# Optimization experiments

Measured on AMD Instinct MI355X. Metric: run time of the kernel, lower is better.

The kernel has to match this reference:

```python
import jax, jax.numpy as jnp
import numpy as np

L = 14  # max_relative_position
H = 12  # num_heads
HD = 64  # head_dim


def rel_pos_embed(N, table_v, table_h):
    # 2D relative-position embedding with a leading CLS token (index 0).
    n = N - 1
    s = int(n ** 0.5)  # grid side (14)
    r = jnp.arange(n)
    dv = r[None, :] // s - r[:, None] // s  # vertical distance
    dh = r[None, :] % s - r[:, None] % s   # horizontal distance
    iv = jnp.clip(dv, -L, L) + L + 1
    ih = jnp.clip(dh, -L, L) + L + 1
    iv = jnp.pad(iv, ((1, 0), (1, 0)))  # CLS row/col -> index 0
    ih = jnp.pad(ih, ((1, 0), (1, 0)))
    return table_v[iv] + table_h[ih]  # [N, N, HD]


def setup_inputs() -> dict:
    key = jax.random.key(0)
    ks = jax.random.split(key, 11)
    B, N, E = 64, 197, 768
    T = 2 * L + 2  # rel-pos table rows (30)
    std = 0.02
    return {
        "x": jax.random.normal(ks[0], (B, N, E), jnp.float32),
        "wq": jax.random.normal(ks[1], (E, H * HD), jnp.float32) * std,
        "wk": jax.random.normal(ks[2], (E, H * HD), jnp.float32) * std,
        "wv": jax.random.normal(ks[3], (E, H * HD), jnp.float32) * std,
        "wproj": jax.random.normal(ks[4], (H * HD, E), jnp.float32) * std,
        "bproj": jnp.zeros((E,), jnp.float32),
        "rk_v": jax.random.normal(ks[5], (T, HD), jnp.float32) * std,
        "rk_h": jax.random.normal(ks[6], (T, HD), jnp.float32) * std,
        "rv_v": jax.random.normal(ks[7], (T, HD), jnp.float32) * std,
        "rv_h": jax.random.normal(ks[8], (T, HD), jnp.float32) * std,
    }


def reference(x, wq, wk, wv, wproj, bproj, rk_v, rk_h, rv_v, rv_h):
    B, N, E = x.shape
    scale = HD ** -0.5
    q = (x @ wq).reshape(B, N, H, HD).transpose(0, 2, 1, 3)  # [B,H,N,HD]
    k = (x @ wk).reshape(B, N, H, HD).transpose(0, 2, 1, 3)
    v = (x @ wv).reshape(B, N, H, HD).transpose(0, 2, 1, 3)

    attn = jnp.einsum('bhid,bhjd->bhij', q, k) * scale
    rpk = rel_pos_embed(N, rk_v, rk_h)  # [N,N,HD]
    attn = attn + jnp.einsum('bhid,ijd->bhij', q, rpk) * scale
    attn = jax.nn.softmax(attn, axis=-1)

    out = jnp.einsum('bhij,bhjd->bhid', attn, v)
    rpv = rel_pos_embed(N, rv_v, rv_h)
    out = out + jnp.einsum('bhij,ijd->bhid', attn, rpv)

    out = out.transpose(0, 2, 1, 3).reshape(B, N, H * HD)
    return out @ wproj + bproj
```

## Files before the change

### kernel.cpp

```cpp
#include <hip/hip_runtime.h>
#include <math.h>

typedef _Float16 f16;
typedef __attribute__((ext_vector_type(8))) _Float16 f16x8;
typedef __attribute__((ext_vector_type(4))) _Float16 f16x4;
typedef __attribute__((ext_vector_type(4))) float f32x4;

#define NH 12
#define HDIM 64
#define NTOK 197
#define EDIM 768
#define NB 64
#define MROWS (NB*NTOK)

__device__ __forceinline__ void wfence() {
    asm volatile("s_waitcnt lgkmcnt(0)" ::: "memory");
    __builtin_amdgcn_sched_barrier(0);
    __builtin_amdgcn_wave_barrier();
}

__device__ __forceinline__ unsigned div14(unsigned n) { return (n * 4682u) >> 16; }

__device__ __forceinline__ void gload16(const f16* g, f16* lds_base) {
    __builtin_amdgcn_global_load_lds(
        (const __attribute__((address_space(1))) void*)g,
        (__attribute__((address_space(3))) void*)lds_base, 16, 0, 0);
}

__global__ __launch_bounds__(256) void prep_all(
    const float* __restrict__ x,
    const float* __restrict__ wq, const float* __restrict__ wk,
    const float* __restrict__ wv, const float* __restrict__ wp,
    const float* __restrict__ rkv, const float* __restrict__ rkh,
    f16* __restrict__ xh, f16* __restrict__ wqkvT, f16* __restrict__ wpT,
    f16* __restrict__ gA, f16* __restrict__ gt_buf)
{
    __shared__ float T[64][65];
    const int bid = blockIdx.x;
    if (bid < 4728) {
        int idx = bid * 256 + threadIdx.x;
        const float4* s = (const float4*)x + (size_t)idx * 2;
        float4 a = s[0], b = s[1];
        f16x8 h;
        h[0]=(f16)a.x; h[1]=(f16)a.y; h[2]=(f16)a.z; h[3]=(f16)a.w;
        h[4]=(f16)b.x; h[5]=(f16)b.y; h[6]=(f16)b.z; h[7]=(f16)b.w;
        *(f16x8*)(xh + (size_t)idx * 8) = h;
    } else if (bid < 5304) {
        int b2 = bid - 4728;
        int m = b2 / 144, rem = b2 - m*144;
        const float* src = (m==0)?wq:(m==1)?wk:(m==2)?wv:wp;
        int k0 = (rem / 12) * 64, n0 = (rem % 12) * 64;
        int cidx = threadIdx.x & 63, r4 = threadIdx.x >> 6;
#pragma unroll
        for (int rr = 0; rr < 16; ++rr) {
            int kl = rr*4 + r4;
            T[kl][cidx] = src[(size_t)(k0+kl)*EDIM + n0 + cidx];
        }
        __syncthreads();
        f16* dst = (m < 3) ? (wqkvT + (size_t)m*EDIM*EDIM) : wpT;
#pragma unroll
        for (int rr = 0; rr < 16; ++rr) {
            int nl = rr*4 + r4;
            dst[(size_t)(n0+nl)*EDIM + k0 + cidx] = (f16)T[cidx][nl];
        }
    } else {
        int t = (bid - 5304) * 256 + threadIdx.x;
        const int stride = 32 * 256;
        for (int i = t; i < 272*128; i += stride) {
            int row = i >> 7, cs = i & 127;
            int c = cs ^ ((row & 7) << 3);
            f16 v = (f16)0.f;
            if (c < 64) {
                if (row >= 208 && row < 238)      v = (f16)rkv[(row-208)*64 + c];
                else if (row >= 240 && row < 270) v = (f16)rkh[(row-240)*64 + c];
            } else if (c < 96 && row < 208) {
                int g = c - 64;
                if (row == 0) { if (g == 14 || g == 30) v = (f16)1.f; }
                else if (row <= 196) {
                    int rm = row - 1;
                    int gv = (int)div14((unsigned)rm), gh = rm - gv*14;
                    if (g == gv || g == 16 + gh) v = (f16)1.f;
                }
            }
            gA[i] = v;
        }
        for (int i = t; i < 32*256; i += stride) {
            int g = i >> 8, cs = i & 255;
            int j = cs ^ ((g & 7) << 3);
            f16 v = (f16)0.f;
            if (j >= 1 && j <= 196) {
                int jm = j - 1;
                int gv = (int)div14((unsigned)jm), gh = jm - gv*14;
                if ((g < 14 && gv == g) || (g >= 16 && g < 30 && gh == g - 16))
                    v = (f16)1.f;
            }
            gt_buf[i] = v;
        }
    }
}

__global__ __launch_bounds__(512, 2) void gemm256(
    const f16* __restrict__ A, const f16* __restrict__ Bt,
    f16* __restrict__ q_o, f16* __restrict__ k_o, f16* __restrict__ v_o,
    float* __restrict__ p_o, const float* __restrict__ bias, int mode, int nxb)
{
    __shared__ f16 lds[2*16384];

    const int tid = threadIdx.x;
    const int l = tid & 63, w = tid >> 6;
    const int lr = l & 15, lq = l >> 4;
    const int wr = w >> 2, wc = w & 3;

    const int nwg = gridDim.x, orig = blockIdx.x;
    const int xcd = orig & 7, qc = nwg >> 3, rc = nwg & 7;
    const int wgid = (xcd < rc ? xcd*(qc+1) : rc*(qc+1) + (xcd-rc)*qc) + (orig >> 3);
    const int mband = wgid / nxb, nband = wgid - mband*nxb;
    const int m0 = mband << 8, n0 = nband << 8;

    const int scol = (((tid & 7) ^ ((tid >> 3) & 7)) << 3);
    const f16* aG[4]; const f16* bG[4];
#pragma unroll
    for (int p = 0; p < 4; ++p) {
        int rt = p*64 + (tid >> 3);
        int ra = m0 + rt; if (ra >= MROWS) ra = MROWS - 1;
        aG[p] = A  + (size_t)ra * EDIM + scol;
        bG[p] = Bt + (size_t)(n0 + rt) * EDIM + scol;
    }
    const int lbase = w * 512;

    f32x4 acc[8][4];
#pragma unroll
    for (int mt = 0; mt < 8; ++mt)
#pragma unroll
        for (int nt = 0; nt < 4; ++nt) {
            acc[mt][nt][0]=0.f; acc[mt][nt][1]=0.f;
            acc[mt][nt][2]=0.f; acc[mt][nt][3]=0.f;
        }

#pragma unroll
    for (int p = 0; p < 4; ++p) {
        gload16(aG[p], &lds[p*4096 + lbase]);
        gload16(bG[p], &lds[16384 + p*4096 + lbase]);
    }
    asm volatile("s_waitcnt vmcnt(0)" ::: "memory");
    __builtin_amdgcn_sched_barrier(0);
    __builtin_amdgcn_s_barrier();

    const int swz = (lr & 7) << 3;
    for (int kt = 0; kt < 12; ++kt) {
        __builtin_amdgcn_s_setprio(1);
#pragma unroll
        for (int ks = 0; ks < 2; ++ks) {
            const int kb = (ks*32 + lq*8) ^ swz;
            f16x8 bf[4];
#pragma unroll
            for (int nt = 0; nt < 4; ++nt)
                bf[nt] = *(const f16x8*)&lds[16384 + (wc*64 + nt*16 + lr)*64 + kb];
#pragma unroll
            for (int mt = 0; mt < 8; ++mt) {
                f16x8 af = *(const f16x8*)&lds[(wr*128 + mt*16 + lr)*64 + kb];
#pragma unroll
                for (int nt = 0; nt < 4; ++nt)
                    acc[mt][nt] = __builtin_amdgcn_mfma_f32_16x16x32_f16(
                        af, bf[nt], acc[mt][nt], 0, 0, 0);
            }
        }
        __builtin_amdgcn_s_setprio(0);
        __builtin_amdgcn_s_barrier();
        if (kt < 11) {
            const int ko = (kt + 1) * 64;
#pragma unroll
            for (int p = 0; p < 4; ++p) {
                gload16(aG[p] + ko, &lds[p*4096 + lbase]);
                gload16(bG[p] + ko, &lds[16384 + p*4096 + lbase]);
            }
            asm volatile("s_waitcnt vmcnt(0)" ::: "memory");
            __builtin_amdgcn_sched_barrier(0);
            __builtin_amdgcn_s_barrier();
        }
    }

    if (mode == 0) {
        const int mat   = n0 / EDIM;
        const int hbase = ((n0 % EDIM) >> 6) + wc;
        f16* dst = (mat == 0) ? q_o : (mat == 1) ? k_o : v_o;
        f16* scr = &lds[w * 2304];
#pragma unroll
        for (int mt2 = 0; mt2 < 4; ++mt2) {
#pragma unroll
            for (int mtp = 0; mtp < 2; ++mtp) {
                const int mt = mt2*2 + mtp;
#pragma unroll
                for (int nt = 0; nt < 4; ++nt)
#pragma unroll
                    for (int rg = 0; rg < 4; ++rg)
                        scr[(mtp*16 + lq*4 + rg)*72 + nt*16 + lr] = (f16)acc[mt][nt][rg];
            }
            wfence();
#pragma unroll
            for (int i = 0; i < 4; ++i) {
                int row = (l >> 3) + i*8;
                f16x8 v = *(const f16x8*)&scr[row*72 + (l & 7)*8];
                int R = m0 + wr*128 + mt2*32 + row;
                if (R < MROWS) {
                    int bb = R / NTOK, nn = R - bb*NTOK;
                    *(f16x8*)&dst[((size_t)(bb*NH + hbase)*NTOK + nn)*HDIM + (l & 7)*8] = v;
                }
            }
            wfence();
        }
    } else {
#pragma unroll
        for (int mt = 0; mt < 8; ++mt)
#pragma unroll
            for (int rg = 0; rg < 4; ++rg) {
                int R = m0 + wr*128 + mt*16 + lq*4 + rg;
                if (R < MROWS) {
                    float* base = p_o + (size_t)R * EDIM + n0 + wc*64;
#pragma unroll
                    for (int nt = 0; nt < 4; ++nt) {
                        int c = nt*16 + lr;
                        base[c] = acc[mt][nt][rg] + bias[n0 + wc*64 + c];
                    }
                }
            }
    }
}

#define SKE 128
#define SVT 320
#define SGT 256
#define SWS 72
#define ATHR 832

__global__ __launch_bounds__(ATHR, 1) void attn_mfma(
    const f16* __restrict__ q_ws, const f16* __restrict__ k_ws,
    const f16* __restrict__ v_ws,
    const float* __restrict__ rvv, const float* __restrict__ rvh,
    const f16* __restrict__ gA, const f16* __restrict__ gt_buf,
    f16* __restrict__ o_ws)
{
    __shared__ f16 Kle[272*SKE];
    __shared__ f16 Vt[64*SVT];
    __shared__ f16 Gt[32*SGT];
    __shared__ f16 WSh[13*16*SWS];

    const int tid = threadIdx.x;
    const int w = tid >> 6, l = tid & 63;
    const int lr = l & 15, lq = l >> 4;
    const int bh = blockIdx.x;
    const int b = bh / NH, h = bh - b * NH;
    const f16* Qp = q_ws + (size_t)bh * NTOK * HDIM;
    const f16* Kp = k_ws + (size_t)bh * NTOK * HDIM;
    const f16* Vp = v_ws + (size_t)bh * NTOK * HDIM;
    f16* wsh = &WSh[w * 16 * SWS];

    for (int c = w; c < 84; c += 13) {
        f16* ldsb;
        const f16* gsrc;
        if (c < 68) {
            int idx = c*64 + l;
            int row = idx >> 4, cs8 = (idx & 15) << 3;
            ldsb = &Kle[c * 512];
            gsrc = (row < NTOK && cs8 < 64)
                 ? (Kp + row*64 + (cs8 ^ ((row & 7) << 3)))
                 : (gA + row*SKE + cs8);
        } else {
            int c2 = c - 68;
            ldsb = &Gt[c2 * 512];
            gsrc = gt_buf + c2*512 + l*8;
        }
        gload16(gsrc, ldsb);
    }

    f16x8 vbuf[4];
#pragma unroll
    for (int it = 0; it < 4; ++it) {
        int idx = tid + it*ATHR;
        if (idx < 8*SVT) {
            int dlow = idx & 7, k = idx >> 3;
            bool isV = (k < NTOK), isA = (k >= 208 && k < 238), isB = (k >= 238 && k < 268);
#pragma unroll
            for (int e = 0; e < 8; ++e) {
                int d = (e << 3) + dlow;
                f16 val = (f16)0.f;
                if (isV)      val = Vp[k*64 + d];
                else if (isA) val = (f16)rvv[(k-208)*64 + d];
                else if (isB) val = (f16)rvh[(k-238)*64 + d];
                vbuf[it][e] = val;
            }
        }
    }

    const int tt = w;
    const int i0 = tt * 16;
    const int iq = i0 + lr;
    const int iqc = (iq > 196) ? 196 : iq;
    const f16* qsrc = Qp + iqc*64 + lq*8;
    f16x8 qf0 = *(const f16x8*)qsrc;
    f16x8 qf1 = *(const f16x8*)(qsrc + 32);

    __syncthreads();

    const int src0 = ((l >> 4) & 1) * 32 + lr;
    const int src1 = src0 + 16;
    const int sw = (lr & 7) << 3;

    {
        __builtin_amdgcn_s_setprio(1);
        f32x4 pacc[4];
#pragma unroll
        for (int ct = 0; ct < 4; ++ct) {
            f32x4 a; a[0]=0.f; a[1]=0.f; a[2]=0.f; a[3]=0.f;
            const int krow = (13+ct)*16 + lr;
            f16x8 kf0 = *(f16x8*)&Kle[krow*SKE + ((lq*8) ^ sw)];
            f16x8 kf1 = *(f16x8*)&Kle[krow*SKE + ((32 + lq*8) ^ sw)];
            a = __builtin_amdgcn_mfma_f32_16x16x32_f16(kf0, qf0, a, 0, 0, 0);
            a = __builtin_amdgcn_mfma_f32_16x16x32_f16(kf1, qf1, a, 0, 0, 0);
            pacc[ct] = a;
        }
        __builtin_amdgcn_s_setprio(0);
#pragma unroll
        for (int ct = 0; ct < 4; ++ct)
#pragma unroll
            for (int rg = 0; rg < 4; ++rg)
                wsh[lr*SWS + ct*16 + lq*4 + rg] = (f16)pacc[ct][rg];
        wfence();

        int id_ = 0, ih_ = 0;
        const bool qcls = (iq == 0);
        if (iq > 0) { unsigned v = div14((unsigned)(iq-1)); id_ = (int)v; ih_ = (iq-1) - (int)v*14; }
        f16x8 qcf;
#pragma unroll
        for (int e = 0; e < 8; ++e) {
            int g = lq*8 + e;
            int toff;
            if (g < 14)       toff = qcls ? 0 : (g - id_ + 15);
            else if (g == 14) toff = 0;
            else if (g == 15) toff = 63;
            else if (g < 30)  toff = qcls ? 32 : (32 + (g-16) - ih_ + 15);
            else if (g == 30) toff = 32;
            else              toff = 63;
            qcf[e] = wsh[lr*SWS + toff];
        }

        f32x4 acc[13];
        __builtin_amdgcn_s_setprio(1);
#pragma unroll
        for (int ct = 0; ct < 13; ++ct) {
            f32x4 a; a[0]=0.f; a[1]=0.f; a[2]=0.f; a[3]=0.f;
            const int krow = ct*16 + lr;
            f16x8 kf0 = *(f16x8*)&Kle[krow*SKE + ((lq*8) ^ sw)];
            f16x8 kf1 = *(f16x8*)&Kle[krow*SKE + ((32 + lq*8) ^ sw)];
            f16x8 gf  = *(f16x8*)&Kle[krow*SKE + ((64 + lq*8) ^ sw)];
            a = __builtin_amdgcn_mfma_f32_16x16x32_f16(kf0, qf0, a, 0, 0, 0);
            a = __builtin_amdgcn_mfma_f32_16x16x32_f16(kf1, qf1, a, 0, 0, 0);
            a = __builtin_amdgcn_mfma_f32_16x16x32_f16(gf,  qcf, a, 0, 0, 0);
            acc[ct] = a;
        }
        __builtin_amdgcn_s_setprio(0);

#pragma unroll
        for (int rg = 0; rg < 4; ++rg)
            if (lq*4 + rg > 4) acc[12][rg] = -1e30f;

        float m = -1e30f;
#pragma unroll
        for (int ct = 0; ct < 13; ++ct)
#pragma unroll
            for (int rg = 0; rg < 4; ++rg) m = fmaxf(m, acc[ct][rg]);
        m = fmaxf(m, __shfl_xor(m, 16));
        m = fmaxf(m, __shfl_xor(m, 32));
        const float C1 = 0.125f * 1.44269504088896f;
        const float nm = -m * C1;
        float ssum = 0.f;
#pragma unroll
        for (int ct = 0; ct < 13; ++ct)
#pragma unroll
            for (int rg = 0; rg < 4; ++rg) {
                float p = exp2f(fmaf(acc[ct][rg], C1, nm));
                acc[ct][rg] = p; ssum += p;
            }
        ssum += __shfl_xor(ssum, 16);
        ssum += __shfl_xor(ssum, 32);
        const float inv = 1.f / ssum;
        const float pn00 = acc[0][0] * inv;

        unsigned pk[13][2];
#pragma unroll
        for (int ct = 0; ct < 13; ++ct) {
            union { f16x4 hh; unsigned u[2]; } t;
            t.hh[0] = (f16)(acc[ct][0] * inv);
            t.hh[1] = (f16)(acc[ct][1] * inv);
            t.hh[2] = (f16)(acc[ct][2] * inv);
            t.hh[3] = (f16)(acc[ct][3] * inv);
            pk[ct][0] = t.u[0]; pk[ct][1] = t.u[1];
        }

        f16x8 pa[7];
#pragma unroll
        for (int kc = 0; kc < 7; ++kc) {
            const int ctA = 2*kc;
            const int ctB = (kc == 6) ? 12 : 2*kc + 1;
            unsigned A0 = (unsigned)__shfl((int)pk[ctA][0], src0);
            unsigned A1 = (unsigned)__shfl((int)pk[ctA][1], src0);
            unsigned A2 = (unsigned)__shfl((int)pk[ctA][0], src1);
            unsigned A3 = (unsigned)__shfl((int)pk[ctA][1], src1);
            unsigned B0 = (unsigned)__shfl((int)pk[ctB][0], src0);
            unsigned B1 = (unsigned)__shfl((int)pk[ctB][1], src0);
            unsigned B2 = (unsigned)__shfl((int)pk[ctB][0], src1);
            unsigned B3 = (unsigned)__shfl((int)pk[ctB][1], src1);
            bool hiHalf = (lq >= 2);
            union { unsigned u[4]; f16x8 v; } f;
            f.u[0] = hiHalf ? B0 : A0;
            f.u[1] = hiHalf ? B1 : A1;
            f.u[2] = hiHalf ? B2 : A2;
            f.u[3] = hiHalf ? B3 : A3;
            if (kc == 6 && hiHalf) { f.u[0]=0; f.u[1]=0; f.u[2]=0; f.u[3]=0; }
            pa[kc] = f.v;
        }

        f32x4 gacc[2];
#pragma unroll
        for (int ct = 0; ct < 2; ++ct) { gacc[ct][0]=0.f; gacc[ct][1]=0.f; gacc[ct][2]=0.f; gacc[ct][3]=0.f; }
        __builtin_amdgcn_s_setprio(1);
#pragma unroll
        for (int kc = 0; kc < 7; ++kc) {
#pragma unroll
            for (int ct = 0; ct < 2; ++ct) {
                f16x8 gf = *(f16x8*)&Gt[(ct*16 + lr)*SGT + ((kc*32 + lq*8) ^ sw)];
                gacc[ct] = __builtin_amdgcn_mfma_f32_16x16x32_f16(pa[kc], gf, gacc[ct], 0, 0, 0);
            }
        }
        __builtin_amdgcn_s_setprio(0);

#pragma unroll
        for (int z = 0; z < 2; ++z) {
            int zi = z*64 + l;
            int zr = zi >> 3, zc = (zi & 7) << 3;
            f16x8 zz;
#pragma unroll
            for (int e = 0; e < 8; ++e) zz[e] = (f16)0.f;
            *(f16x8*)&wsh[zr*SWS + zc] = zz;
        }
        wfence();
#pragma unroll
        for (int rg = 0; rg < 4; ++rg) {
            int il = lq*4 + rg;
            int is_ = i0 + il;
            if (lr < 14 && is_ > 0) {
                unsigned v = div14((unsigned)(is_-1));
                int id2 = (int)v, ih2 = (is_-1) - (int)v*14;
                wsh[il*SWS + (lr - id2 + 15)]      = (f16)gacc[0][rg];
                wsh[il*SWS + 30 + (lr - ih2 + 15)] = (f16)gacc[1][rg];
            }
        }
        if (lq == 0 && !(i0 == 0 && lr == 0)) {
            wsh[lr*SWS + 0]  = (f16)pn00;
            wsh[lr*SWS + 30] = (f16)pn00;
        }
        if (i0 == 0) {
            float sv = (lq == 0) ? gacc[0][0] : 0.f;
            float sh = (lq == 0) ? gacc[1][0] : 0.f;
            sv += __shfl_xor(sv, 1); sv += __shfl_xor(sv, 2);
            sv += __shfl_xor(sv, 4); sv += __shfl_xor(sv, 8);
            sh += __shfl_xor(sh, 1); sh += __shfl_xor(sh, 2);
            sh += __shfl_xor(sh, 4); sh += __shfl_xor(sh, 8);
            if (l == 0) {
                wsh[0]  = (f16)(sv + pn00);
                wsh[30] = (f16)(sh + pn00);
            }
        }
        wfence();

#pragma unroll
        for (int it = 0; it < 4; ++it) {
            int idx = tid + it*ATHR;
            if (idx < 8*SVT) {
                int dlow = idx & 7, k = idx >> 3;
                int kx = k ^ (dlow << 3);
#pragma unroll
                for (int e = 0; e < 8; ++e)
                    Vt[((e << 3) + dlow)*SVT + kx] = vbuf[it][e];
            }
        }
        __syncthreads();

        f16x8 sfr[2];
#pragma unroll
        for (int kc2 = 0; kc2 < 2; ++kc2)
            sfr[kc2] = *(f16x8*)&wsh[lr*SWS + kc2*32 + lq*8];

        f32x4 oacc[4];
#pragma unroll
        for (int ct = 0; ct < 4; ++ct) { oacc[ct][0]=0.f; oacc[ct][1]=0.f; oacc[ct][2]=0.f; oacc[ct][3]=0.f; }
        __builtin_amdgcn_s_setprio(1);
#pragma unroll
        for (int kc = 0; kc < 7; ++kc) {
#pragma unroll
            for (int ct = 0; ct < 4; ++ct) {
                f16x8 vf = *(f16x8*)&Vt[(ct*16 + lr)*SVT + ((kc*32 + lq*8) ^ sw)];
                oacc[ct] = __builtin_amdgcn_mfma_f32_16x16x32_f16(pa[kc], vf, oacc[ct], 0, 0, 0);
            }
        }
#pragma unroll
        for (int kc2 = 0; kc2 < 2; ++kc2) {
#pragma unroll
            for (int ct = 0; ct < 4; ++ct) {
                f16x8 vf = *(f16x8*)&Vt[(ct*16 + lr)*SVT + ((208 + kc2*32 + lq*8) ^ sw)];
                oacc[ct] = __builtin_amdgcn_mfma_f32_16x16x32_f16(sfr[kc2], vf, oacc[ct], 0, 0, 0);
            }
        }
        __builtin_amdgcn_s_setprio(0);

#pragma unroll
        for (int ct = 0; ct < 4; ++ct)
#pragma unroll
            for (int rg = 0; rg < 4; ++rg) {
                int io = i0 + lq*4 + rg;
                if (io < NTOK) {
                    int d = ct*16 + lr;
                    o_ws[((size_t)(b * NTOK + io) * NH + h) * HDIM + d] = (f16)oacc[ct][rg];
                }
            }
    }
}

extern "C" void kernel_launch(void* const* d_in, const int* in_sizes, int n_in,
                              void* d_out, int out_size, void* d_ws, size_t ws_size,
                              hipStream_t stream)
{
    const float* x     = (const float*)d_in[0];
    const float* wq    = (const float*)d_in[1];
    const float* wk    = (const float*)d_in[2];
    const float* wv    = (const float*)d_in[3];
    const float* wproj = (const float*)d_in[4];
    const float* bproj = (const float*)d_in[5];
    const float* rkv   = (const float*)d_in[6];
    const float* rkh   = (const float*)d_in[7];
    const float* rvv   = (const float*)d_in[8];
    const float* rvh   = (const float*)d_in[9];

    f16* ws = (f16*)d_ws;
    const size_t sz = (size_t)MROWS * EDIM;
    f16* xh    = ws;
    f16* qh    = xh + sz;
    f16* kh    = qh + sz;
    f16* vh    = kh + sz;
    f16* oh    = vh + sz;
    f16* wqkvT = oh + sz;
    f16* wpT   = wqkvT + (size_t)3*EDIM*EDIM;
    f16* gA    = wpT   + (size_t)EDIM*EDIM;
    f16* gtb   = gA    + 272*128;

    prep_all<<<5336, 256, 0, stream>>>(x, wq, wk, wv, wproj, rkv, rkh,
                                       xh, wqkvT, wpT, gA, gtb);
    gemm256 <<<50*9, 512, 0, stream>>>(xh, wqkvT, qh, kh, vh,
                                       nullptr, nullptr, 0, 9);
    attn_mfma<<<NB * NH, ATHR, 0, stream>>>(qh, kh, vh,
                                            rvv, rvh, gA, gtb, oh);
    gemm256 <<<50*3, 512, 0, stream>>>(oh, wpT, nullptr, nullptr, nullptr,
                                       (float*)d_out, bproj, 1, 3);
}
```

Baseline: 161.1 us.

## Triple-buffer GEMM K-loop and shrink N-tile to 128 for more workgroups

```diff
diff --git a/kernel.cpp b/kernel.cpp
--- a/kernel.cpp
+++ b/kernel.cpp
@@ -104,50 +104,63 @@
     f16* __restrict__ q_o, f16* __restrict__ k_o, f16* __restrict__ v_o,
     float* __restrict__ p_o, const float* __restrict__ bias, int mode, int nxb)
 {
-    __shared__ f16 lds[2*16384];
+    __shared__ f16 lds[73728];
 
     const int tid = threadIdx.x;
     const int l = tid & 63, w = tid >> 6;
     const int lr = l & 15, lq = l >> 4;
-    const int wr = w >> 2, wc = w & 3;
+    const int wr = w >> 1, wc = w & 1;
 
     const int nwg = gridDim.x, orig = blockIdx.x;
     const int xcd = orig & 7, qc = nwg >> 3, rc = nwg & 7;
     const int wgid = (xcd < rc ? xcd*(qc+1) : rc*(qc+1) + (xcd-rc)*qc) + (orig >> 3);
     const int mband = wgid / nxb, nband = wgid - mband*nxb;
-    const int m0 = mband << 8, n0 = nband << 8;
+    const int m0 = mband << 8, n0 = nband << 7;
 
     const int scol = (((tid & 7) ^ ((tid >> 3) & 7)) << 3);
-    const f16* aG[4]; const f16* bG[4];
+    const f16* aG[4]; const f16* bG[2];
 #pragma unroll
     for (int p = 0; p < 4; ++p) {
         int rt = p*64 + (tid >> 3);
         int ra = m0 + rt; if (ra >= MROWS) ra = MROWS - 1;
-        aG[p] = A  + (size_t)ra * EDIM + scol;
+        aG[p] = A + (size_t)ra * EDIM + scol;
+    }
+#pragma unroll
+    for (int p = 0; p < 2; ++p) {
+        int rt = p*64 + (tid >> 3);
         bG[p] = Bt + (size_t)(n0 + rt) * EDIM + scol;
     }
     const int lbase = w * 512;
 
-    f32x4 acc[8][4];
-#pragma unroll
-    for (int mt = 0; mt < 8; ++mt)
+#define STAGE(T) { const int ab_ = ((T)%3)*16384, bb_ = 49152 + ((T)%3)*8192; \
+        const int ko_ = (T)*64; \
+        gload16(aG[0] + ko_, &lds[ab_ + 0*4096 + lbase]); \
+        gload16(aG[1] + ko_, &lds[ab_ + 1*4096 + lbase]); \
+        gload16(aG[2] + ko_, &lds[ab_ + 2*4096 + lbase]); \
+        gload16(aG[3] + ko_, &lds[ab_ + 3*4096 + lbase]); \
+        gload16(bG[0] + ko_, &lds[bb_ + 0*4096 + lbase]); \
+        gload16(bG[1] + ko_, &lds[bb_ + 1*4096 + lbase]); }
+
+    f32x4 acc[4][4];
+#pragma unroll
+    for (int mt = 0; mt < 4; ++mt)
 #pragma unroll
         for (int nt = 0; nt < 4; ++nt) {
             acc[mt][nt][0]=0.f; acc[mt][nt][1]=0.f;
             acc[mt][nt][2]=0.f; acc[mt][nt][3]=0.f;
         }
 
-#pragma unroll
-    for (int p = 0; p < 4; ++p) {
-        gload16(aG[p], &lds[p*4096 + lbase]);
-        gload16(bG[p], &lds[16384 + p*4096 + lbase]);
-    }
-    asm volatile("s_waitcnt vmcnt(0)" ::: "memory");
+    STAGE(0); STAGE(1);
+    asm volatile("s_waitcnt vmcnt(6)" ::: "memory");
     __builtin_amdgcn_sched_barrier(0);
     __builtin_amdgcn_s_barrier();
 
     const int swz = (lr & 7) << 3;
-    for (int kt = 0; kt < 12; ++kt) {
+    for (int it = 0; it < 12; ++it) {
+        if (it + 2 < 12) STAGE(it + 2);
+        __builtin_amdgcn_sched_barrier(0);
+        const f16* Ab = &lds[(it % 3) * 16384];
+        const f16* Bb = &lds[49152 + (it % 3) * 8192];
         __builtin_amdgcn_s_setprio(1);
 #pragma unroll
         for (int ks = 0; ks < 2; ++ks) {
@@ -155,10 +168,10 @@
             f16x8 bf[4];
 #pragma unroll
             for (int nt = 0; nt < 4; ++nt)
-                bf[nt] = *(const f16x8*)&lds[16384 + (wc*64 + nt*16 + lr)*64 + kb];
-#pragma unroll
-            for (int mt = 0; mt < 8; ++mt) {
-                f16x8 af = *(const f16x8*)&lds[(wr*128 + mt*16 + lr)*64 + kb];
+                bf[nt] = *(const f16x8*)&Bb[(wc*64 + nt*16 + lr)*64 + kb];
+#pragma unroll
+            for (int mt = 0; mt < 4; ++mt) {
+                f16x8 af = *(const f16x8*)&Ab[(wr*64 + mt*16 + lr)*64 + kb];
 #pragma unroll
                 for (int nt = 0; nt < 4; ++nt)
                     acc[mt][nt] = __builtin_amdgcn_mfma_f32_16x16x32_f16(
@@ -166,19 +179,13 @@
             }
         }
         __builtin_amdgcn_s_setprio(0);
+        if (it < 10)      asm volatile("s_waitcnt vmcnt(6)" ::: "memory");
+        else if (it == 10) asm volatile("s_waitcnt vmcnt(0)" ::: "memory");
+        __builtin_amdgcn_sched_barrier(0);
         __builtin_amdgcn_s_barrier();
-        if (kt < 11) {
-            const int ko = (kt + 1) * 64;
-#pragma unroll
-            for (int p = 0; p < 4; ++p) {
-                gload16(aG[p] + ko, &lds[p*4096 + lbase]);
-                gload16(bG[p] + ko, &lds[16384 + p*4096 + lbase]);
-            }
-            asm volatile("s_waitcnt vmcnt(0)" ::: "memory");
-            __builtin_amdgcn_sched_barrier(0);
-            __builtin_amdgcn_s_barrier();
-        }
-    }
+    }
+#undef STAGE
+    __syncthreads();
 
     if (mode == 0) {
         const int mat   = n0 / EDIM;
@@ -186,7 +193,7 @@
         f16* dst = (mat == 0) ? q_o : (mat == 1) ? k_o : v_o;
         f16* scr = &lds[w * 2304];
 #pragma unroll
-        for (int mt2 = 0; mt2 < 4; ++mt2) {
+        for (int mt2 = 0; mt2 < 2; ++mt2) {
 #pragma unroll
             for (int mtp = 0; mtp < 2; ++mtp) {
                 const int mt = mt2*2 + mtp;
@@ -201,7 +208,7 @@
             for (int i = 0; i < 4; ++i) {
                 int row = (l >> 3) + i*8;
                 f16x8 v = *(const f16x8*)&scr[row*72 + (l & 7)*8];
-                int R = m0 + wr*128 + mt2*32 + row;
+                int R = m0 + wr*64 + mt2*32 + row;
                 if (R < MROWS) {
                     int bb = R / NTOK, nn = R - bb*NTOK;
                     *(f16x8*)&dst[((size_t)(bb*NH + hbase)*NTOK + nn)*HDIM + (l & 7)*8] = v;
@@ -211,10 +218,10 @@
         }
     } else {
 #pragma unroll
-        for (int mt = 0; mt < 8; ++mt)
+        for (int mt = 0; mt < 4; ++mt)
 #pragma unroll
             for (int rg = 0; rg < 4; ++rg) {
-                int R = m0 + wr*128 + mt*16 + lq*4 + rg;
+                int R = m0 + wr*64 + mt*16 + lq*4 + rg;
                 if (R < MROWS) {
                     float* base = p_o + (size_t)R * EDIM + n0 + wc*64;
 #pragma unroll
@@ -555,10 +562,10 @@
 
     prep_all<<<5336, 256, 0, stream>>>(x, wq, wk, wv, wproj, rkv, rkh,
                                        xh, wqkvT, wpT, gA, gtb);
-    gemm256 <<<50*9, 512, 0, stream>>>(xh, wqkvT, qh, kh, vh,
-                                       nullptr, nullptr, 0, 9);
+    gemm256 <<<50*18, 512, 0, stream>>>(xh, wqkvT, qh, kh, vh,
+                                        nullptr, nullptr, 0, 18);
     attn_mfma<<<NB * NH, ATHR, 0, stream>>>(qh, kh, vh,
                                             rvv, rvh, gA, gtb, oh);
-    gemm256 <<<50*3, 512, 0, stream>>>(oh, wpT, nullptr, nullptr, nullptr,
-                                       (float*)d_out, bproj, 1, 3);
+    gemm256 <<<50*6, 512, 0, stream>>>(oh, wpT, nullptr, nullptr, nullptr,
+                                       (float*)d_out, bproj, 1, 6);
 }
```

Measured after the change: 167.6 us. 1.04x slower.

## Double-buffer GEMM LDS tiles with staged half-tile prefetch interleaved into MFMA quadrants

Applied to the files above, without the earlier changes.

```diff
diff --git a/kernel.cpp b/kernel.cpp
--- a/kernel.cpp
+++ b/kernel.cpp
@@ -104,7 +104,7 @@
     f16* __restrict__ q_o, f16* __restrict__ k_o, f16* __restrict__ v_o,
     float* __restrict__ p_o, const float* __restrict__ bias, int mode, int nxb)
 {
-    __shared__ f16 lds[2*16384];
+    __shared__ f16 lds[4*16384];
 
     const int tid = threadIdx.x;
     const int l = tid & 63, w = tid >> 6;
@@ -117,16 +117,29 @@
     const int mband = wgid / nxb, nband = wgid - mband*nxb;
     const int m0 = mband << 8, n0 = nband << 8;
 
-    const int scol = (((tid & 7) ^ ((tid >> 3) & 7)) << 3);
-    const f16* aG[4]; const f16* bG[4];
-#pragma unroll
-    for (int p = 0; p < 4; ++p) {
-        int rt = p*64 + (tid >> 3);
-        int ra = m0 + rt; if (ra >= MROWS) ra = MROWS - 1;
-        aG[p] = A  + (size_t)ra * EDIM + scol;
-        bG[p] = Bt + (size_t)(n0 + rt) * EDIM + scol;
-    }
-    const int lbase = w * 512;
+    const int scol2 = (((l & 7) ^ (l >> 3)) << 3);
+    const f16* aC[2][2]; const f16* bC[2][2];
+    int aRT[2][2], bRT[2][2];
+#pragma unroll
+    for (int H = 0; H < 2; ++H)
+#pragma unroll
+        for (int cc = 0; cc < 2; ++cc) {
+            int c_ = w*2 + cc;
+            int art = (c_ >> 3)*128 + H*64 + (c_ & 7)*8;
+            int ra = m0 + art + (l >> 3); if (ra >= MROWS) ra = MROWS - 1;
+            aC[H][cc] = A + (size_t)ra * EDIM + scol2;
+            aRT[H][cc] = art;
+            int brt = (c_ >> 2)*64 + H*32 + (c_ & 3)*8;
+            bC[H][cc] = Bt + (size_t)(n0 + brt + (l >> 3)) * EDIM + scol2;
+            bRT[H][cc] = brt;
+        }
+
+#define STAGE_AH(T, H) { const int bb_ = ((T)&1)*16384; const int ko_ = (T)*64; \
+        gload16(aC[H][0] + ko_, &lds[bb_ + aRT[H][0]*64]); \
+        gload16(aC[H][1] + ko_, &lds[bb_ + aRT[H][1]*64]); }
+#define STAGE_BH(T, H) { const int bb_ = 32768 + ((T)&1)*16384; const int ko_ = (T)*64; \
+        gload16(bC[H][0] + ko_, &lds[bb_ + bRT[H][0]*64]); \
+        gload16(bC[H][1] + ko_, &lds[bb_ + bRT[H][1]*64]); }
 
     f32x4 acc[8][4];
 #pragma unroll
@@ -137,48 +150,57 @@
             acc[mt][nt][2]=0.f; acc[mt][nt][3]=0.f;
         }
 
-#pragma unroll
-    for (int p = 0; p < 4; ++p) {
-        gload16(aG[p], &lds[p*4096 + lbase]);
-        gload16(bG[p], &lds[16384 + p*4096 + lbase]);
-    }
-    asm volatile("s_waitcnt vmcnt(0)" ::: "memory");
+    STAGE_AH(0,0); STAGE_AH(0,1); STAGE_BH(0,0); STAGE_BH(0,1);
+    STAGE_AH(1,0); STAGE_BH(1,0);
+    asm volatile("s_waitcnt vmcnt(4)" ::: "memory");
     __builtin_amdgcn_sched_barrier(0);
     __builtin_amdgcn_s_barrier();
 
     const int swz = (lr & 7) << 3;
-    for (int kt = 0; kt < 12; ++kt) {
-        __builtin_amdgcn_s_setprio(1);
-#pragma unroll
-        for (int ks = 0; ks < 2; ++ks) {
-            const int kb = (ks*32 + lq*8) ^ swz;
-            f16x8 bf[4];
-#pragma unroll
-            for (int nt = 0; nt < 4; ++nt)
-                bf[nt] = *(const f16x8*)&lds[16384 + (wc*64 + nt*16 + lr)*64 + kb];
-#pragma unroll
-            for (int mt = 0; mt < 8; ++mt) {
-                f16x8 af = *(const f16x8*)&lds[(wr*128 + mt*16 + lr)*64 + kb];
-#pragma unroll
-                for (int nt = 0; nt < 4; ++nt)
-                    acc[mt][nt] = __builtin_amdgcn_mfma_f32_16x16x32_f16(
-                        af, bf[nt], acc[mt][nt], 0, 0, 0);
-            }
-        }
-        __builtin_amdgcn_s_setprio(0);
-        __builtin_amdgcn_s_barrier();
-        if (kt < 11) {
-            const int ko = (kt + 1) * 64;
-#pragma unroll
-            for (int p = 0; p < 4; ++p) {
-                gload16(aG[p] + ko, &lds[p*4096 + lbase]);
-                gload16(bG[p] + ko, &lds[16384 + p*4096 + lbase]);
-            }
-            asm volatile("s_waitcnt vmcnt(0)" ::: "memory");
+    for (int it = 0; it < 12; ++it) {
+        const f16* Ab = &lds[(it & 1) * 16384];
+        const f16* Bb = &lds[32768 + (it & 1) * 16384];
+#pragma unroll
+        for (int q = 0; q < 4; ++q) {
+            const int mq = q >> 1, nq = q & 1;
+            f16x8 af[4][2], bf[2][2];
+#pragma unroll
+            for (int ks = 0; ks < 2; ++ks) {
+                const int kb = (ks*32 + lq*8) ^ swz;
+#pragma unroll
+                for (int mt = 0; mt < 4; ++mt)
+                    af[mt][ks] = *(const f16x8*)&Ab[(wr*128 + mq*64 + mt*16 + lr)*64 + kb];
+#pragma unroll
+                for (int nt = 0; nt < 2; ++nt)
+                    bf[nt][ks] = *(const f16x8*)&Bb[(wc*64 + nq*32 + nt*16 + lr)*64 + kb];
+            }
+            if (q == 0)      { if (it + 1 < 12) STAGE_AH(it+1, 1); }
+            else if (q == 1) { if (it + 1 < 12) STAGE_BH(it+1, 1); }
+            else if (q == 2) { if (it + 2 < 12) STAGE_AH(it+2, 0); }
+            else             { if (it + 2 < 12) STAGE_BH(it+2, 0); }
+            __builtin_amdgcn_s_barrier();
+            asm volatile("s_waitcnt lgkmcnt(0)" ::: "memory");
             __builtin_amdgcn_sched_barrier(0);
+            __builtin_amdgcn_s_setprio(1);
+#pragma unroll
+            for (int ks = 0; ks < 2; ++ks)
+#pragma unroll
+                for (int mt = 0; mt < 4; ++mt)
+#pragma unroll
+                    for (int nt = 0; nt < 2; ++nt)
+                        acc[mq*4 + mt][nq*2 + nt] = __builtin_amdgcn_mfma_f32_16x16x32_f16(
+                            af[mt][ks], bf[nt][ks], acc[mq*4 + mt][nq*2 + nt], 0, 0, 0);
+            __builtin_amdgcn_s_setprio(0);
+            if (q == 3) {
+                if (it < 10) asm volatile("s_waitcnt vmcnt(4)" ::: "memory");
+                else         asm volatile("s_waitcnt vmcnt(0)" ::: "memory");
+                __builtin_amdgcn_sched_barrier(0);
+            }
             __builtin_amdgcn_s_barrier();
         }
     }
+#undef STAGE_AH
+#undef STAGE_BH
 
     if (mode == 0) {
         const int mat   = n0 / EDIM;
```

New measurement: 151.8 us. 5.8% less time.
